# Kernel optimization log

Hardware: AMD Instinct MI355X
Metric: run time of the kernel (lower is better)

The kernel has to match this reference:

```python
import jax, jax.numpy as jnp
import numpy as np

HEAD_CHOICES = [8, 10, 12]
MAX_HEADS = 12
HEAD_DIM = 64
MAX_REL_POS = 14
SCALE = HEAD_DIM ** -0.5


def _rel_indices(N):
    # AutoFormer RelativePosition2D_super index computation (static, numpy).
    L = N - 1                      # remove cls token
    s = int(L ** 0.5)              # patches per row
    r = np.arange(L)
    dv = r[None, :] // s - r[:, None] // s
    dh = r[None, :] % s - r[:, None] % s
    iv = np.clip(dv, -MAX_REL_POS, MAX_REL_POS) + MAX_REL_POS + 1
    ih = np.clip(dh, -MAX_REL_POS, MAX_REL_POS) + MAX_REL_POS + 1
    iv = np.pad(iv, ((1, 0), (1, 0)))  # cls token row/col -> index 0
    ih = np.pad(ih, ((1, 0), (1, 0)))
    return jnp.asarray(iv), jnp.asarray(ih)


def setup_inputs() -> dict:
    key = jax.random.key(0)
    ks = jax.random.split(key, 6)
    B, N = 16, 577
    T = 2 * MAX_REL_POS + 2  # 30
    x = jax.random.normal(ks[0], (B, N, 3 * MAX_HEADS * HEAD_DIM), dtype=jnp.float32)
    weights = jax.nn.softmax(jax.random.normal(ks[1], (len(HEAD_CHOICES),), dtype=jnp.float32))
    rel_k_table_v = jax.random.normal(ks[2], (T, HEAD_DIM), dtype=jnp.float32) * 0.02
    rel_k_table_h = jax.random.normal(ks[3], (T, HEAD_DIM), dtype=jnp.float32) * 0.02
    rel_v_table_v = jax.random.normal(ks[4], (T, HEAD_DIM), dtype=jnp.float32) * 0.02
    rel_v_table_h = jax.random.normal(ks[5], (T, HEAD_DIM), dtype=jnp.float32) * 0.02
    return dict(x=x, weights=weights,
                rel_k_table_v=rel_k_table_v, rel_k_table_h=rel_k_table_h,
                rel_v_table_v=rel_v_table_v, rel_v_table_h=rel_v_table_h)


def reference(x, weights, rel_k_table_v, rel_k_table_h, rel_v_table_v, rel_v_table_h):
    B, N, _ = x.shape
    # [3, B, H, N, D]
    qkv = x.reshape(B, N, 3, MAX_HEADS, HEAD_DIM).transpose(2, 0, 3, 1, 4)
    # Mixture over head-count choices: slicing first c heads, scaling by w[i],
    # padding to max_heads, and summing == per-head weight sum_i w[i]*[h < c_i].
    head_mask = jnp.asarray(np.array([[1.0 if h < c else 0.0 for h in range(MAX_HEADS)]
                                      for c in HEAD_CHOICES]), dtype=x.dtype)  # [C, H]
    w_head = weights @ head_mask  # [H]
    w4 = w_head[None, :, None, None]
    q = qkv[0] * w4
    k = qkv[1] * w4
    v = qkv[2] * w4
    # content attention + relative-position K bias
    attn = jnp.einsum('bhnd,bhmd->bhnm', q, k) * SCALE
    iv, ih = _rel_indices(N)
    rel_k = rel_k_table_v[iv] + rel_k_table_h[ih]  # [N, N, D]
    attn = attn + jnp.einsum('bhnd,nmd->bhnm', q, rel_k) * SCALE
    attn = jax.nn.softmax(attn, axis=-1)  # attn_drop has p=0 (eval)
    out = jnp.einsum('bhnm,bhmd->bhnd', attn, v)
    rel_v = rel_v_table_v[iv] + rel_v_table_h[ih]  # [N, N, D]
    out = out + jnp.einsum('bhnm,nmd->bhnd', attn, rel_v)
    return out.transpose(0, 2, 1, 3).reshape(B, N, MAX_HEADS * HEAD_DIM)
```

## Files before the change

kernel.cpp:

```cpp
#include <hip/hip_runtime.h>

typedef short bf16x8_t __attribute__((ext_vector_type(8)));
typedef float f32x4_t __attribute__((ext_vector_type(4)));

#define NTOK 577
#define NPAD 608
#define VPAD 640
#define NSTEP 19

__device__ __forceinline__ unsigned short f2bf(float f) {
  unsigned u = __builtin_bit_cast(unsigned, f);
  u += 0x7FFFu + ((u >> 16) & 1u);
  return (unsigned short)(u >> 16);
}
__device__ __forceinline__ float headw(const float* wts, int h) {
  float w0 = wts[0], w1 = wts[1], w2 = wts[2];
  return (h < 8) ? (w0 + w1 + w2) : ((h < 10) ? (w1 + w2) : w2);
}
__device__ __forceinline__ unsigned rangemask(int lo, int hi) {
  lo = lo < 0 ? 0 : lo; hi = hi > 32 ? 32 : hi;
  if (hi <= lo) return 0u;
  unsigned mh = (hi >= 32) ? 0xFFFFFFFFu : ((1u << hi) - 1u);
  unsigned ml = (1u << lo) - 1u;
  return mh & ~ml;
}

extern "C" __global__ __launch_bounds__(256) void prep_qk(
    const float* __restrict__ x, const float* __restrict__ wts,
    unsigned short* __restrict__ qbf, unsigned short* __restrict__ kbf) {
  int tid = threadIdx.x;
  int cid = blockIdx.x * 256 + tid;
  int d4 = cid & 15, n = cid >> 4;
  int h = blockIdx.y >> 1, sel = blockIdx.y & 1;
  int b = blockIdx.z;
  float w = headw(wts, h);
  float scale = sel ? 1.f : (w * w * 0.125f);
  float4 v = make_float4(0.f, 0.f, 0.f, 0.f);
  if (n < NTOK) v = *(const float4*)(x + ((size_t)(b * NTOK + n)) * 2304 + sel * 768 + h * 64 + d4 * 4);
  ushort4 o;
  o.x = f2bf(v.x * scale); o.y = f2bf(v.y * scale);
  o.z = f2bf(v.z * scale); o.w = f2bf(v.w * scale);
  unsigned short* base = sel ? kbf : qbf;
  *(ushort4*)(base + (((size_t)(b * 12 + h)) * NPAD + n) * 64 + d4 * 4) = o;
}

extern "C" __global__ __launch_bounds__(256) void prep_v(
    const float* __restrict__ x, unsigned short* __restrict__ vbf) {
  __shared__ unsigned short t_s[64][72];
  int tid = threadIdx.x;
  int n0 = blockIdx.x * 64, h = blockIdx.y, b = blockIdx.z;
  for (int p = 0; p < 4; ++p) {
    int c = p * 256 + tid;
    int ni = c >> 4, d4 = c & 15;
    int n = n0 + ni;
    float4 v = make_float4(0.f, 0.f, 0.f, 0.f);
    if (n < NTOK) v = *(const float4*)(x + ((size_t)(b * NTOK + n)) * 2304 + 1536 + h * 64 + d4 * 4);
    t_s[d4 * 4 + 0][ni] = f2bf(v.x);
    t_s[d4 * 4 + 1][ni] = f2bf(v.y);
    t_s[d4 * 4 + 2][ni] = f2bf(v.z);
    t_s[d4 * 4 + 3][ni] = f2bf(v.w);
  }
  __syncthreads();
  for (int p = 0; p < 2; ++p) {
    int c = p * 256 + tid;
    int d = c >> 3, n8 = c & 7;
    bf16x8_t val = *(const bf16x8_t*)&t_s[d][n8 * 8];
    *(bf16x8_t*)(vbf + ((size_t)(b * 12 + h) * 64 + d) * VPAD + n0 + n8 * 8) = val;
  }
}

extern "C" __global__ __launch_bounds__(256) void prep_tab(
    const float* __restrict__ wts,
    const float* __restrict__ tkv, const float* __restrict__ tkh,
    const float* __restrict__ tvv, const float* __restrict__ tvh,
    unsigned short* __restrict__ tkb, unsigned short* __restrict__ tvb) {
  int tid = threadIdx.x, bx = blockIdx.x;
  if (bx < 48) {
    int cid = bx * 256 + tid;
    int d4 = cid & 15, t = (cid >> 4) & 31, tb = (cid >> 9) & 1, h = cid >> 10;
    float s = 1.f / headw(wts, h);
    const float* src = tb ? tkh : tkv;
    float4 v = make_float4(0.f, 0.f, 0.f, 0.f);
    if (t < 30) v = *(const float4*)(src + t * 64 + d4 * 4);
    ushort4 o;
    o.x = f2bf(v.x * s); o.y = f2bf(v.y * s); o.z = f2bf(v.z * s); o.w = f2bf(v.w * s);
    *(ushort4*)(tkb + (((size_t)(h * 2 + tb)) * 32 + t) * 64 + d4 * 4) = o;
  } else {
    for (int i = 0; i < 16; ++i) {
      int id = tid * 16 + i;
      int t = id & 31, d = (id >> 5) & 63, tb = id >> 11;
      const float* src = tb ? tvh : tvv;
      tvb[id] = (t < 30) ? f2bf(src[t * 64 + d]) : (unsigned short)0;
    }
  }
}

struct __align__(16) SMem {
  unsigned short q_s[32][72];
  float qg_s[2][32][25];
  unsigned gmask_s[2][NSTEP][25];
  union {
    struct { float qv_t[2][32][32]; } pro;
    struct {
      unsigned short k_s[32][72];
      unsigned short v_sT[64][40];
      unsigned short P_s[32][40];
    } loop;
    struct {
      float sv_f[2][32][30];
      unsigned short sv_bf[2][32][32];
      float l_s[32];
    } epi;
  } u;
};

extern "C" __global__ __launch_bounds__(256, 6) void hma_kernel(
    const unsigned short* __restrict__ qbf, const unsigned short* __restrict__ kbf,
    const unsigned short* __restrict__ vbf, const unsigned short* __restrict__ tkb,
    const unsigned short* __restrict__ tvb, const float* __restrict__ wts,
    float* __restrict__ out) {
  __shared__ SMem sm;
  const int tid = threadIdx.x;
  const int wave = tid >> 6, lane = tid & 63, quad = lane >> 4, l15 = lane & 15;
  const int rg = wave & 1, cg = wave >> 1, tb_w = wave >> 1;
  const int n0 = blockIdx.x * 32;
  const int h = blockIdx.y, b = blockIdx.z;
  const float w = headw(wts, h);

  const unsigned short* qb = qbf + ((size_t)(b * 12 + h)) * NPAD * 64;
  const unsigned short* kb = kbf + ((size_t)(b * 12 + h)) * NPAD * 64;
  const unsigned short* vb = vbf + ((size_t)(b * 12 + h)) * 64 * VPAD;

  {
    int row = tid >> 3, ch = tid & 7;
    bf16x8_t v = *(const bf16x8_t*)(qb + (size_t)(n0 + row) * 64 + ch * 8);
    *(bf16x8_t*)&sm.q_s[row][ch * 8] = v;
  }
  for (int p = tid; p < 2 * NSTEP * 25; p += 256) {
    int tb = p / (NSTEP * 25), r2 = p % (NSTEP * 25), step = r2 / 25, g = r2 % 25;
    int m0 = step * 32;
    unsigned mask;
    if (g == 24) {
      mask = rangemask(NTOK - m0, NPAD - m0);
      if (step == 0) mask |= 1u;
    } else if (tb == 0) {
      mask = rangemask(24 * g + 1 - m0, 24 * g + 25 - m0);
    } else {
      mask = 0u;
      int j0 = (g + 1 - m0) % 24; if (j0 < 0) j0 += 24;
      for (int j = j0; j < 32; j += 24) {
        int m = m0 + j;
        if (m >= 1 && m < NTOK) mask |= (1u << j);
      }
    }
    sm.gmask_s[tb][step][g] = mask;
  }
  __syncthreads();
  {
    const unsigned short* tkp = tkb + ((size_t)(h * 2 + tb_w)) * 32 * 64;
    for (int tt = 0; tt < 2; ++tt) {
      f32x4_t acc = {0.f, 0.f, 0.f, 0.f};
      for (int kk = 0; kk < 2; ++kk) {
        bf16x8_t a = *(const bf16x8_t*)&sm.q_s[rg * 16 + l15][kk * 32 + quad * 8];
        bf16x8_t bb = *(const bf16x8_t*)(tkp + (size_t)(tt * 16 + l15) * 64 + kk * 32 + quad * 8);
        acc = __builtin_amdgcn_mfma_f32_16x16x32_bf16(a, bb, acc, 0, 0, 0);
      }
      for (int r = 0; r < 4; ++r)
        sm.u.pro.qv_t[tb_w][rg * 16 + quad * 4 + r][tt * 16 + l15] = acc[r];
    }
  }
  __syncthreads();
  for (int p = tid; p < 2 * 32 * 25; p += 256) {
    int tb = p / 800, r2 = p % 800, n = r2 / 25, g = r2 % 25;
    int n_g = n0 + n;
    int t;
    if (n_g == 0 || n_g >= NTOK || g == 24) t = 0;
    else {
      int base = tb ? ((n_g - 1) % 24) : ((n_g - 1) / 24);
      int dq = g - base; dq = dq < -14 ? -14 : (dq > 14 ? 14 : dq);
      t = dq + 15;
    }
    sm.qg_s[tb][n][g] = sm.u.pro.qv_t[tb][n][t];
  }

  const int m_loc = cg * 16 + l15;
  int rmv, cmv;
  if (m_loc == 0) { rmv = 0; cmv = -1; }
  else { rmv = (m_loc - 1) / 24; cmv = (m_loc - 1) - rmv * 24; }
  const bool cls_lane = (m_loc == 0);

  f32x4_t oacc[2] = {{0,0,0,0},{0,0,0,0}};
  f32x4_t rsacc[2] = {{0,0,0,0},{0,0,0,0}};

  const int krow = tid >> 3, kch = tid & 7;
  const int vrow = tid >> 2, vch = tid & 3;
  const unsigned short* kptr = kb + (size_t)krow * 64 + kch * 8;
  const unsigned short* vptr = vb + (size_t)vrow * VPAD + vch * 8;
  bf16x8_t kreg = *(const bf16x8_t*)kptr;
  bf16x8_t vreg = *(const bf16x8_t*)vptr;

  for (int step = 0; step < NSTEP; ++step) {
    const int m0 = step * 32;
    __syncthreads();
    *(bf16x8_t*)&sm.u.loop.k_s[krow][kch * 8] = kreg;
    *(bf16x8_t*)&sm.u.loop.v_sT[vrow][vch * 8] = vreg;
    __syncthreads();
    if (step < NSTEP - 1) {
      kreg = *(const bf16x8_t*)(kptr + (size_t)(m0 + 32) * 64);
      vreg = *(const bf16x8_t*)(vptr + (m0 + 32));
    }
    f32x4_t s = {0.f, 0.f, 0.f, 0.f};
    for (int kk = 0; kk < 2; ++kk) {
      bf16x8_t a = *(const bf16x8_t*)&sm.q_s[rg * 16 + l15][kk * 32 + quad * 8];
      bf16x8_t bb = *(const bf16x8_t*)&sm.u.loop.k_s[cg * 16 + l15][kk * 32 + quad * 8];
      s = __builtin_amdgcn_mfma_f32_16x16x32_bf16(a, bb, s, 0, 0, 0);
    }
    const int m_g = m0 + m_loc;
    int ur = rmv, uc = cmv;
    if (cls_lane && step == 0) { ur = 24; uc = 24; }
    const bool mpad = (m_g >= NTOK);
    for (int r = 0; r < 4; ++r) {
      int n_loc = rg * 16 + quad * 4 + r;
      float logit = s[r] + sm.qg_s[0][n_loc][ur] + sm.qg_s[1][n_loc][uc];
      float p = __expf(logit);
      if (mpad) p = 0.f;
      unsigned u = __builtin_bit_cast(unsigned, p);
      sm.u.loop.P_s[n_loc][m_loc] = (unsigned short)((u + 0x8000u) >> 16);
    }
    { int c = cmv + 8; int carry = (c >= 24); cmv = carry ? c - 24 : c; rmv += 1 + carry; }
    __syncthreads();
    bf16x8_t a = *(const bf16x8_t*)&sm.u.loop.P_s[rg * 16 + l15][quad * 8];
    for (int sub = 0; sub < 2; ++sub) {
      bf16x8_t bb = *(const bf16x8_t*)&sm.u.loop.v_sT[cg * 32 + sub * 16 + l15][quad * 8];
      oacc[sub] = __builtin_amdgcn_mfma_f32_16x16x32_bf16(a, bb, oacc[sub], 0, 0, 0);
    }
    for (int gt = 0; gt < 2; ++gt) {
      unsigned g = (unsigned)(gt * 16 + l15);
      unsigned mask = (g < 25) ? sm.gmask_s[tb_w][step][g] : 0u;
      unsigned bits = (mask >> (quad * 8)) & 0xFFu;
      unsigned y0 = ((bits & 0xFu) * 0x204081u) & 0x01010101u;
      unsigned y1 = ((bits >> 4) * 0x204081u) & 0x01010101u;
      unsigned p01 = y0 & 0x0101u, p23 = (y0 >> 16) & 0x0101u;
      unsigned p45 = y1 & 0x0101u, p67 = (y1 >> 16) & 0x0101u;
      union { unsigned uu[4]; bf16x8_t v; } gbu;
      gbu.uu[0] = ((p01 | (p01 << 8)) & 0x00010001u) * 0x3F80u;
      gbu.uu[1] = ((p23 | (p23 << 8)) & 0x00010001u) * 0x3F80u;
      gbu.uu[2] = ((p45 | (p45 << 8)) & 0x00010001u) * 0x3F80u;
      gbu.uu[3] = ((p67 | (p67 << 8)) & 0x00010001u) * 0x3F80u;
      rsacc[gt] = __builtin_amdgcn_mfma_f32_16x16x32_bf16(a, gbu.v, rsacc[gt], 0, 0, 0);
    }
  }

  __syncthreads();
  for (int e = tid; e < 2 * 32 * 30; e += 256) (&sm.u.epi.sv_f[0][0][0])[e] = 0.f;
  __syncthreads();
  {
    int n_loc4 = rg * 16 + quad * 4;
    for (int gt = 0; gt < 2; ++gt) {
      int g = gt * 16 + l15;
      if (g < 25) {
        for (int r = 0; r < 4; ++r) {
          int n_g = n0 + n_loc4 + r;
          int t;
          if (n_g == 0 || n_g >= NTOK || g == 24) t = 0;
          else {
            int base = tb_w ? ((n_g - 1) % 24) : ((n_g - 1) / 24);
            int dq = g - base; dq = dq < -14 ? -14 : (dq > 14 ? 14 : dq);
            t = dq + 15;
          }
          atomicAdd(&sm.u.epi.sv_f[tb_w][n_loc4 + r][t], rsacc[gt][r]);
        }
      }
    }
  }
  __syncthreads();
  if (tid < 32) {
    float l = 0.f;
    for (int t = 0; t < 30; ++t) l += sm.u.epi.sv_f[0][tid][t];
    sm.u.epi.l_s[tid] = l;
  }
  for (int e = tid; e < 2048; e += 256) {
    int tb = e >> 10, r2 = e & 1023, n = r2 >> 5, t = r2 & 31;
    float v = (t < 30) ? sm.u.epi.sv_f[tb][n][t] : 0.f;
    unsigned u = __builtin_bit_cast(unsigned, v);
    sm.u.epi.sv_bf[tb][n][t] = (unsigned short)((u + 0x8000u) >> 16);
  }
  for (int sub = 0; sub < 2; ++sub)
    for (int r = 0; r < 4; ++r) oacc[sub][r] *= w;
  __syncthreads();
  for (int tb = 0; tb < 2; ++tb) {
    bf16x8_t a = *(const bf16x8_t*)&sm.u.epi.sv_bf[tb][rg * 16 + l15][quad * 8];
    for (int sub = 0; sub < 2; ++sub) {
      bf16x8_t bb = *(const bf16x8_t*)(tvb + ((size_t)(tb * 64 + cg * 32 + sub * 16 + l15)) * 32 + quad * 8);
      oacc[sub] = __builtin_amdgcn_mfma_f32_16x16x32_bf16(a, bb, oacc[sub], 0, 0, 0);
    }
  }
  float* ob = out + (size_t)b * NTOK * 768 + h * 64;
  for (int r = 0; r < 4; ++r) {
    int n_loc = rg * 16 + quad * 4 + r;
    int n_g = n0 + n_loc;
    if (n_g < NTOK) {
      float inv = 1.f / sm.u.epi.l_s[n_loc];
      for (int sub = 0; sub < 2; ++sub) {
        int d = cg * 32 + sub * 16 + l15;
        ob[(size_t)n_g * 768 + d] = oacc[sub][r] * inv;
      }
    }
  }
}

extern "C" void kernel_launch(void* const* d_in, const int* in_sizes, int n_in,
                              void* d_out, int out_size, void* d_ws, size_t ws_size,
                              hipStream_t stream) {
  const float* x   = (const float*)d_in[0];
  const float* wts = (const float*)d_in[1];
  const float* tkv = (const float*)d_in[2];
  const float* tkh = (const float*)d_in[3];
  const float* tvv = (const float*)d_in[4];
  const float* tvh = (const float*)d_in[5];
  float* out = (float*)d_out;
  const int B = in_sizes[0] / (NTOK * 2304);

  unsigned short* ws = (unsigned short*)d_ws;
  size_t qkSz = (size_t)B * 12 * NPAD * 64;
  size_t vSz  = (size_t)B * 12 * 64 * VPAD;
  unsigned short* qbf = ws;
  unsigned short* kbf = ws + qkSz;
  unsigned short* vbf = ws + 2 * qkSz;
  unsigned short* tkb = vbf + vSz;
  unsigned short* tvb = tkb + (size_t)12 * 2 * 32 * 64;

  prep_qk<<<dim3(38, 24, B), 256, 0, stream>>>(x, wts, qbf, kbf);
  prep_v<<<dim3(10, 12, B), 256, 0, stream>>>(x, vbf);
  prep_tab<<<dim3(49, 1, 1), 256, 0, stream>>>(wts, tkv, tkh, tvv, tvh, tkb, tvb);
  hma_kernel<<<dim3(NSTEP, 12, B), 256, 0, stream>>>(qbf, kbf, vbf, tkb, tvb, wts, out);
}
```

Baseline: 295.0 us.

## Widen query tile to 64 rows, keep Q in registers, fuse prep kernels

The attention kernel now handles 64 query rows per block instead of 32. Each wave keeps two 16-row Q fragments in registers, so every K/V tile loaded into shared memory is reused across twice as many queries and the Q shared buffer goes away. The separate Q/K and V prep kernels are merged into one pass over x, and the epilogue converts the bias sums to bf16 in registers instead of through shared memory. In exchange the kernel uses more registers and shared memory (occupancy hint lowered from 6 to 5) and launches half as many blocks, which may underfill the GPU.

```diff
diff --git a/kernel.cpp b/kernel.cpp
--- a/kernel.cpp
+++ b/kernel.cpp
@@ -4,8 +4,8 @@
 typedef float f32x4_t __attribute__((ext_vector_type(4)));
 
 #define NTOK 577
-#define NPAD 608
-#define VPAD 640
+#define QPAD 640
+#define MPAD 608
 #define NSTEP 19
 
 __device__ __forceinline__ unsigned short f2bf(float f) {
@@ -25,47 +25,45 @@
   return mh & ~ml;
 }
 
-extern "C" __global__ __launch_bounds__(256) void prep_qk(
+extern "C" __global__ __launch_bounds__(256) void prep_x(
     const float* __restrict__ x, const float* __restrict__ wts,
-    unsigned short* __restrict__ qbf, unsigned short* __restrict__ kbf) {
-  int tid = threadIdx.x;
-  int cid = blockIdx.x * 256 + tid;
-  int d4 = cid & 15, n = cid >> 4;
-  int h = blockIdx.y >> 1, sel = blockIdx.y & 1;
-  int b = blockIdx.z;
-  float w = headw(wts, h);
-  float scale = sel ? 1.f : (w * w * 0.125f);
-  float4 v = make_float4(0.f, 0.f, 0.f, 0.f);
-  if (n < NTOK) v = *(const float4*)(x + ((size_t)(b * NTOK + n)) * 2304 + sel * 768 + h * 64 + d4 * 4);
-  ushort4 o;
-  o.x = f2bf(v.x * scale); o.y = f2bf(v.y * scale);
-  o.z = f2bf(v.z * scale); o.w = f2bf(v.w * scale);
-  unsigned short* base = sel ? kbf : qbf;
-  *(ushort4*)(base + (((size_t)(b * 12 + h)) * NPAD + n) * 64 + d4 * 4) = o;
-}
-
-extern "C" __global__ __launch_bounds__(256) void prep_v(
-    const float* __restrict__ x, unsigned short* __restrict__ vbf) {
+    unsigned short* __restrict__ qbf, unsigned short* __restrict__ kbf,
+    unsigned short* __restrict__ vbf) {
   __shared__ unsigned short t_s[64][72];
-  int tid = threadIdx.x;
-  int n0 = blockIdx.x * 64, h = blockIdx.y, b = blockIdx.z;
+  const int tid = threadIdx.x;
+  const int n0 = blockIdx.x * 64, h = blockIdx.y, b = blockIdx.z;
+  const float w = headw(wts, h);
+  const float qs = w * w * 0.125f;
+  const float* xb = x + (size_t)(b * NTOK) * 2304 + h * 64;
+  unsigned short* qo = qbf + ((size_t)(b * 12 + h)) * QPAD * 64;
+  unsigned short* ko = kbf + ((size_t)(b * 12 + h)) * QPAD * 64;
   for (int p = 0; p < 4; ++p) {
-    int c = p * 256 + tid;
-    int ni = c >> 4, d4 = c & 15;
-    int n = n0 + ni;
-    float4 v = make_float4(0.f, 0.f, 0.f, 0.f);
-    if (n < NTOK) v = *(const float4*)(x + ((size_t)(b * NTOK + n)) * 2304 + 1536 + h * 64 + d4 * 4);
-    t_s[d4 * 4 + 0][ni] = f2bf(v.x);
-    t_s[d4 * 4 + 1][ni] = f2bf(v.y);
-    t_s[d4 * 4 + 2][ni] = f2bf(v.z);
-    t_s[d4 * 4 + 3][ni] = f2bf(v.w);
+    int idx = p * 256 + tid;
+    int row = idx >> 4, c4 = idx & 15;
+    int n = n0 + row;
+    float4 vq = {0,0,0,0}, vk = {0,0,0,0}, vv = {0,0,0,0};
+    if (n < NTOK) {
+      const float* rp = xb + (size_t)n * 2304 + c4 * 4;
+      vq = *(const float4*)rp;
+      vk = *(const float4*)(rp + 768);
+      vv = *(const float4*)(rp + 1536);
+    }
+    ushort4 oq, ok;
+    oq.x = f2bf(vq.x * qs); oq.y = f2bf(vq.y * qs); oq.z = f2bf(vq.z * qs); oq.w = f2bf(vq.w * qs);
+    ok.x = f2bf(vk.x); ok.y = f2bf(vk.y); ok.z = f2bf(vk.z); ok.w = f2bf(vk.w);
+    *(ushort4*)(qo + (size_t)(n0 + row) * 64 + c4 * 4) = oq;
+    *(ushort4*)(ko + (size_t)(n0 + row) * 64 + c4 * 4) = ok;
+    t_s[c4 * 4 + 0][row] = f2bf(vv.x);
+    t_s[c4 * 4 + 1][row] = f2bf(vv.y);
+    t_s[c4 * 4 + 2][row] = f2bf(vv.z);
+    t_s[c4 * 4 + 3][row] = f2bf(vv.w);
   }
   __syncthreads();
   for (int p = 0; p < 2; ++p) {
     int c = p * 256 + tid;
     int d = c >> 3, n8 = c & 7;
     bf16x8_t val = *(const bf16x8_t*)&t_s[d][n8 * 8];
-    *(bf16x8_t*)(vbf + ((size_t)(b * 12 + h) * 64 + d) * VPAD + n0 + n8 * 8) = val;
+    *(bf16x8_t*)(vbf + ((size_t)(b * 12 + h) * 64 + d) * QPAD + n0 + n8 * 8) = val;
   }
 }
 
@@ -80,7 +78,7 @@
     int d4 = cid & 15, t = (cid >> 4) & 31, tb = (cid >> 9) & 1, h = cid >> 10;
     float s = 1.f / headw(wts, h);
     const float* src = tb ? tkh : tkv;
-    float4 v = make_float4(0.f, 0.f, 0.f, 0.f);
+    float4 v = {0,0,0,0};
     if (t < 30) v = *(const float4*)(src + t * 64 + d4 * 4);
     ushort4 o;
     o.x = f2bf(v.x * s); o.y = f2bf(v.y * s); o.z = f2bf(v.z * s); o.w = f2bf(v.w * s);
@@ -96,25 +94,21 @@
 }
 
 struct __align__(16) SMem {
-  unsigned short q_s[32][72];
-  float qg_s[2][32][25];
+  float qg_s[2][64][25];
   unsigned gmask_s[2][NSTEP][25];
+  float l_s[64];
   union {
-    struct { float qv_t[2][32][32]; } pro;
+    struct { float qv_t[2][64][30]; } pro;
     struct {
       unsigned short k_s[32][72];
       unsigned short v_sT[64][40];
-      unsigned short P_s[32][40];
+      unsigned short P_s[64][40];
     } loop;
-    struct {
-      float sv_f[2][32][30];
-      unsigned short sv_bf[2][32][32];
-      float l_s[32];
-    } epi;
+    struct { float sv_f[2][64][30]; } epi;
   } u;
 };
 
-extern "C" __global__ __launch_bounds__(256, 6) void hma_kernel(
+extern "C" __global__ __launch_bounds__(256, 5) void hma_kernel(
     const unsigned short* __restrict__ qbf, const unsigned short* __restrict__ kbf,
     const unsigned short* __restrict__ vbf, const unsigned short* __restrict__ tkb,
     const unsigned short* __restrict__ tvb, const float* __restrict__ wts,
@@ -122,26 +116,28 @@
   __shared__ SMem sm;
   const int tid = threadIdx.x;
   const int wave = tid >> 6, lane = tid & 63, quad = lane >> 4, l15 = lane & 15;
-  const int rg = wave & 1, cg = wave >> 1, tb_w = wave >> 1;
-  const int n0 = blockIdx.x * 32;
+  const int rg = wave & 1;
+  const int cg = wave >> 1;
+  const int tb_w = cg;
+  const int n0 = blockIdx.x * 64;
   const int h = blockIdx.y, b = blockIdx.z;
   const float w = headw(wts, h);
 
-  const unsigned short* qb = qbf + ((size_t)(b * 12 + h)) * NPAD * 64;
-  const unsigned short* kb = kbf + ((size_t)(b * 12 + h)) * NPAD * 64;
-  const unsigned short* vb = vbf + ((size_t)(b * 12 + h)) * 64 * VPAD;
-
-  {
-    int row = tid >> 3, ch = tid & 7;
-    bf16x8_t v = *(const bf16x8_t*)(qb + (size_t)(n0 + row) * 64 + ch * 8);
-    *(bf16x8_t*)&sm.q_s[row][ch * 8] = v;
-  }
+  const unsigned short* qb = qbf + ((size_t)(b * 12 + h)) * QPAD * 64;
+  const unsigned short* kb = kbf + ((size_t)(b * 12 + h)) * QPAD * 64;
+  const unsigned short* vb = vbf + ((size_t)(b * 12 + h)) * 64 * QPAD;
+
+  bf16x8_t qa[2][2];
+  for (int sub = 0; sub < 2; ++sub)
+    for (int kk = 0; kk < 2; ++kk)
+      qa[sub][kk] = *(const bf16x8_t*)(qb + (size_t)(n0 + rg * 32 + sub * 16 + l15) * 64 + kk * 32 + quad * 8);
+
   for (int p = tid; p < 2 * NSTEP * 25; p += 256) {
     int tb = p / (NSTEP * 25), r2 = p % (NSTEP * 25), step = r2 / 25, g = r2 % 25;
     int m0 = step * 32;
     unsigned mask;
     if (g == 24) {
-      mask = rangemask(NTOK - m0, NPAD - m0);
+      mask = rangemask(NTOK - m0, MPAD - m0);
       if (step == 0) mask |= 1u;
     } else if (tb == 0) {
       mask = rangemask(24 * g + 1 - m0, 24 * g + 25 - m0);
@@ -155,23 +151,26 @@
     }
     sm.gmask_s[tb][step][g] = mask;
   }
-  __syncthreads();
+
   {
     const unsigned short* tkp = tkb + ((size_t)(h * 2 + tb_w)) * 32 * 64;
     for (int tt = 0; tt < 2; ++tt) {
-      f32x4_t acc = {0.f, 0.f, 0.f, 0.f};
-      for (int kk = 0; kk < 2; ++kk) {
-        bf16x8_t a = *(const bf16x8_t*)&sm.q_s[rg * 16 + l15][kk * 32 + quad * 8];
-        bf16x8_t bb = *(const bf16x8_t*)(tkp + (size_t)(tt * 16 + l15) * 64 + kk * 32 + quad * 8);
-        acc = __builtin_amdgcn_mfma_f32_16x16x32_bf16(a, bb, acc, 0, 0, 0);
-      }
-      for (int r = 0; r < 4; ++r)
-        sm.u.pro.qv_t[tb_w][rg * 16 + quad * 4 + r][tt * 16 + l15] = acc[r];
-    }
-  }
-  __syncthreads();
-  for (int p = tid; p < 2 * 32 * 25; p += 256) {
-    int tb = p / 800, r2 = p % 800, n = r2 / 25, g = r2 % 25;
+      for (int sub = 0; sub < 2; ++sub) {
+        f32x4_t acc = {0.f, 0.f, 0.f, 0.f};
+        for (int kk = 0; kk < 2; ++kk) {
+          bf16x8_t bb = *(const bf16x8_t*)(tkp + (size_t)(tt * 16 + l15) * 64 + kk * 32 + quad * 8);
+          acc = __builtin_amdgcn_mfma_f32_16x16x32_bf16(qa[sub][kk], bb, acc, 0, 0, 0);
+        }
+        int t = tt * 16 + l15;
+        if (t < 30)
+          for (int r = 0; r < 4; ++r)
+            sm.u.pro.qv_t[tb_w][rg * 32 + sub * 16 + quad * 4 + r][t] = acc[r];
+      }
+    }
+  }
+  __syncthreads();
+  for (int p = tid; p < 2 * 64 * 25; p += 256) {
+    int tb = p / 1600, r2 = p % 1600, n = r2 / 25, g = r2 % 25;
     int n_g = n0 + n;
     int t;
     if (n_g == 0 || n_g >= NTOK || g == 24) t = 0;
@@ -189,13 +188,13 @@
   else { rmv = (m_loc - 1) / 24; cmv = (m_loc - 1) - rmv * 24; }
   const bool cls_lane = (m_loc == 0);
 
-  f32x4_t oacc[2] = {{0,0,0,0},{0,0,0,0}};
-  f32x4_t rsacc[2] = {{0,0,0,0},{0,0,0,0}};
+  f32x4_t oacc[2][2] = {{{0,0,0,0},{0,0,0,0}},{{0,0,0,0},{0,0,0,0}}};
+  f32x4_t rsacc[2][2] = {{{0,0,0,0},{0,0,0,0}},{{0,0,0,0},{0,0,0,0}}};
 
   const int krow = tid >> 3, kch = tid & 7;
   const int vrow = tid >> 2, vch = tid & 3;
   const unsigned short* kptr = kb + (size_t)krow * 64 + kch * 8;
-  const unsigned short* vptr = vb + (size_t)vrow * VPAD + vch * 8;
+  const unsigned short* vptr = vb + (size_t)vrow * QPAD + vch * 8;
   bf16x8_t kreg = *(const bf16x8_t*)kptr;
   bf16x8_t vreg = *(const bf16x8_t*)vptr;
 
@@ -205,34 +204,39 @@
     *(bf16x8_t*)&sm.u.loop.k_s[krow][kch * 8] = kreg;
     *(bf16x8_t*)&sm.u.loop.v_sT[vrow][vch * 8] = vreg;
     __syncthreads();
-    if (step < NSTEP - 1) {
-      kreg = *(const bf16x8_t*)(kptr + (size_t)(m0 + 32) * 64);
-      vreg = *(const bf16x8_t*)(vptr + (m0 + 32));
-    }
-    f32x4_t s = {0.f, 0.f, 0.f, 0.f};
-    for (int kk = 0; kk < 2; ++kk) {
-      bf16x8_t a = *(const bf16x8_t*)&sm.q_s[rg * 16 + l15][kk * 32 + quad * 8];
-      bf16x8_t bb = *(const bf16x8_t*)&sm.u.loop.k_s[cg * 16 + l15][kk * 32 + quad * 8];
-      s = __builtin_amdgcn_mfma_f32_16x16x32_bf16(a, bb, s, 0, 0, 0);
+    kreg = *(const bf16x8_t*)(kptr + (size_t)(m0 + 32) * 64);
+    vreg = *(const bf16x8_t*)(vptr + (m0 + 32));
+    f32x4_t s[2] = {{0,0,0,0},{0,0,0,0}};
+    {
+      bf16x8_t kb0 = *(const bf16x8_t*)&sm.u.loop.k_s[cg * 16 + l15][quad * 8];
+      bf16x8_t kb1 = *(const bf16x8_t*)&sm.u.loop.k_s[cg * 16 + l15][32 + quad * 8];
+      for (int sub = 0; sub < 2; ++sub) {
+        s[sub] = __builtin_amdgcn_mfma_f32_16x16x32_bf16(qa[sub][0], kb0, s[sub], 0, 0, 0);
+        s[sub] = __builtin_amdgcn_mfma_f32_16x16x32_bf16(qa[sub][1], kb1, s[sub], 0, 0, 0);
+      }
     }
     const int m_g = m0 + m_loc;
     int ur = rmv, uc = cmv;
     if (cls_lane && step == 0) { ur = 24; uc = 24; }
     const bool mpad = (m_g >= NTOK);
-    for (int r = 0; r < 4; ++r) {
-      int n_loc = rg * 16 + quad * 4 + r;
-      float logit = s[r] + sm.qg_s[0][n_loc][ur] + sm.qg_s[1][n_loc][uc];
-      float p = __expf(logit);
-      if (mpad) p = 0.f;
-      unsigned u = __builtin_bit_cast(unsigned, p);
-      sm.u.loop.P_s[n_loc][m_loc] = (unsigned short)((u + 0x8000u) >> 16);
-    }
+    for (int sub = 0; sub < 2; ++sub)
+      for (int r = 0; r < 4; ++r) {
+        int n_loc = rg * 32 + sub * 16 + quad * 4 + r;
+        float logit = s[sub][r] + sm.qg_s[0][n_loc][ur] + sm.qg_s[1][n_loc][uc];
+        float p = __expf(logit);
+        if (mpad) p = 0.f;
+        unsigned u = __builtin_bit_cast(unsigned, p);
+        sm.u.loop.P_s[n_loc][m_loc] = (unsigned short)((u + 0x8000u) >> 16);
+      }
     { int c = cmv + 8; int carry = (c >= 24); cmv = carry ? c - 24 : c; rmv += 1 + carry; }
     __syncthreads();
-    bf16x8_t a = *(const bf16x8_t*)&sm.u.loop.P_s[rg * 16 + l15][quad * 8];
-    for (int sub = 0; sub < 2; ++sub) {
-      bf16x8_t bb = *(const bf16x8_t*)&sm.u.loop.v_sT[cg * 32 + sub * 16 + l15][quad * 8];
-      oacc[sub] = __builtin_amdgcn_mfma_f32_16x16x32_bf16(a, bb, oacc[sub], 0, 0, 0);
+    bf16x8_t pa[2];
+    for (int sub = 0; sub < 2; ++sub)
+      pa[sub] = *(const bf16x8_t*)&sm.u.loop.P_s[rg * 32 + sub * 16 + l15][quad * 8];
+    for (int ds = 0; ds < 2; ++ds) {
+      bf16x8_t bb = *(const bf16x8_t*)&sm.u.loop.v_sT[cg * 32 + ds * 16 + l15][quad * 8];
+      for (int sub = 0; sub < 2; ++sub)
+        oacc[sub][ds] = __builtin_amdgcn_mfma_f32_16x16x32_bf16(pa[sub], bb, oacc[sub][ds], 0, 0, 0);
     }
     for (int gt = 0; gt < 2; ++gt) {
       unsigned g = (unsigned)(gt * 16 + l15);
@@ -247,20 +251,21 @@
       gbu.uu[1] = ((p23 | (p23 << 8)) & 0x00010001u) * 0x3F80u;
       gbu.uu[2] = ((p45 | (p45 << 8)) & 0x00010001u) * 0x3F80u;
       gbu.uu[3] = ((p67 | (p67 << 8)) & 0x00010001u) * 0x3F80u;
-      rsacc[gt] = __builtin_amdgcn_mfma_f32_16x16x32_bf16(a, gbu.v, rsacc[gt], 0, 0, 0);
-    }
-  }
-
-  __syncthreads();
-  for (int e = tid; e < 2 * 32 * 30; e += 256) (&sm.u.epi.sv_f[0][0][0])[e] = 0.f;
-  __syncthreads();
-  {
-    int n_loc4 = rg * 16 + quad * 4;
+      for (int sub = 0; sub < 2; ++sub)
+        rsacc[sub][gt] = __builtin_amdgcn_mfma_f32_16x16x32_bf16(pa[sub], gbu.v, rsacc[sub][gt], 0, 0, 0);
+    }
+  }
+
+  __syncthreads();
+  for (int e = tid; e < 2 * 64 * 30; e += 256) (&sm.u.epi.sv_f[0][0][0])[e] = 0.f;
+  __syncthreads();
+  for (int sub = 0; sub < 2; ++sub)
     for (int gt = 0; gt < 2; ++gt) {
       int g = gt * 16 + l15;
       if (g < 25) {
         for (int r = 0; r < 4; ++r) {
-          int n_g = n0 + n_loc4 + r;
+          int n_loc = rg * 32 + sub * 16 + quad * 4 + r;
+          int n_g = n0 + n_loc;
           int t;
           if (n_g == 0 || n_g >= NTOK || g == 24) t = 0;
           else {
@@ -268,45 +273,50 @@
             int dq = g - base; dq = dq < -14 ? -14 : (dq > 14 ? 14 : dq);
             t = dq + 15;
           }
-          atomicAdd(&sm.u.epi.sv_f[tb_w][n_loc4 + r][t], rsacc[gt][r]);
+          atomicAdd(&sm.u.epi.sv_f[tb_w][n_loc][t], rsacc[sub][gt][r]);
         }
       }
     }
-  }
-  __syncthreads();
-  if (tid < 32) {
+  __syncthreads();
+  if (tid < 64) {
     float l = 0.f;
     for (int t = 0; t < 30; ++t) l += sm.u.epi.sv_f[0][tid][t];
-    sm.u.epi.l_s[tid] = l;
-  }
-  for (int e = tid; e < 2048; e += 256) {
-    int tb = e >> 10, r2 = e & 1023, n = r2 >> 5, t = r2 & 31;
-    float v = (t < 30) ? sm.u.epi.sv_f[tb][n][t] : 0.f;
-    unsigned u = __builtin_bit_cast(unsigned, v);
-    sm.u.epi.sv_bf[tb][n][t] = (unsigned short)((u + 0x8000u) >> 16);
+    sm.l_s[tid] = l;
   }
   for (int sub = 0; sub < 2; ++sub)
-    for (int r = 0; r < 4; ++r) oacc[sub][r] *= w;
-  __syncthreads();
+    for (int ds = 0; ds < 2; ++ds)
+      for (int r = 0; r < 4; ++r) oacc[sub][ds][r] *= w;
   for (int tb = 0; tb < 2; ++tb) {
-    bf16x8_t a = *(const bf16x8_t*)&sm.u.epi.sv_bf[tb][rg * 16 + l15][quad * 8];
+    bf16x8_t av[2];
     for (int sub = 0; sub < 2; ++sub) {
-      bf16x8_t bb = *(const bf16x8_t*)(tvb + ((size_t)(tb * 64 + cg * 32 + sub * 16 + l15)) * 32 + quad * 8);
-      oacc[sub] = __builtin_amdgcn_mfma_f32_16x16x32_bf16(a, bb, oacc[sub], 0, 0, 0);
-    }
-  }
+      int n_loc = rg * 32 + sub * 16 + l15;
+      for (int j = 0; j < 8; ++j) {
+        int t = quad * 8 + j;
+        float f = (t < 30) ? sm.u.epi.sv_f[tb][n_loc][t] : 0.f;
+        unsigned u = __builtin_bit_cast(unsigned, f);
+        av[sub][j] = (short)((u + 0x8000u) >> 16);
+      }
+    }
+    for (int ds = 0; ds < 2; ++ds) {
+      bf16x8_t bb = *(const bf16x8_t*)(tvb + ((size_t)(tb * 64 + cg * 32 + ds * 16 + l15)) * 32 + quad * 8);
+      for (int sub = 0; sub < 2; ++sub)
+        oacc[sub][ds] = __builtin_amdgcn_mfma_f32_16x16x32_bf16(av[sub], bb, oacc[sub][ds], 0, 0, 0);
+    }
+  }
+  __syncthreads();
   float* ob = out + (size_t)b * NTOK * 768 + h * 64;
-  for (int r = 0; r < 4; ++r) {
-    int n_loc = rg * 16 + quad * 4 + r;
-    int n_g = n0 + n_loc;
-    if (n_g < NTOK) {
-      float inv = 1.f / sm.u.epi.l_s[n_loc];
-      for (int sub = 0; sub < 2; ++sub) {
-        int d = cg * 32 + sub * 16 + l15;
-        ob[(size_t)n_g * 768 + d] = oacc[sub][r] * inv;
-      }
-    }
-  }
+  for (int sub = 0; sub < 2; ++sub)
+    for (int r = 0; r < 4; ++r) {
+      int n_loc = rg * 32 + sub * 16 + quad * 4 + r;
+      int n_g = n0 + n_loc;
+      if (n_g < NTOK) {
+        float inv = 1.f / sm.l_s[n_loc];
+        for (int ds = 0; ds < 2; ++ds) {
+          int d = cg * 32 + ds * 16 + l15;
+          ob[(size_t)n_g * 768 + d] = oacc[sub][ds][r] * inv;
+        }
+      }
+    }
 }
 
 extern "C" void kernel_launch(void* const* d_in, const int* in_sizes, int n_in,
@@ -322,16 +332,14 @@
   const int B = in_sizes[0] / (NTOK * 2304);
 
   unsigned short* ws = (unsigned short*)d_ws;
-  size_t qkSz = (size_t)B * 12 * NPAD * 64;
-  size_t vSz  = (size_t)B * 12 * 64 * VPAD;
+  size_t qkSz = (size_t)B * 12 * QPAD * 64;
   unsigned short* qbf = ws;
   unsigned short* kbf = ws + qkSz;
   unsigned short* vbf = ws + 2 * qkSz;
-  unsigned short* tkb = vbf + vSz;
+  unsigned short* tkb = vbf + qkSz;
   unsigned short* tvb = tkb + (size_t)12 * 2 * 32 * 64;
 
-  prep_qk<<<dim3(38, 24, B), 256, 0, stream>>>(x, wts, qbf, kbf);
-  prep_v<<<dim3(10, 12, B), 256, 0, stream>>>(x, vbf);
+  prep_x<<<dim3(10, 12, B), 256, 0, stream>>>(x, wts, qbf, kbf, vbf);
   prep_tab<<<dim3(49, 1, 1), 256, 0, stream>>>(wts, tkv, tkh, tvv, tvh, tkb, tvb);
-  hma_kernel<<<dim3(NSTEP, 12, B), 256, 0, stream>>>(qbf, kbf, vbf, tkb, tvb, wts, out);
-}
+  hma_kernel<<<dim3(10, 12, B), 256, 0, stream>>>(qbf, kbf, vbf, tkb, tvb, wts, out);
+}
```

New measurement: 274.9 us. 1.07x faster.
